# Kernel tuning notes

Hardware: AMD Instinct MI355X
Metric: run time of the kernel (lower is better)

Reference implementation:

```python
import jax, jax.numpy as jnp
import numpy as np

B, C_IN, H, W = 4, 1536, 64, 64   # SGI input: cat of three 512-ch encoder maps at 64x64
HID, OUT = 1536, 512
N = H * W


def _grid_edge_index(h, w):
    # 4-connected bidirectional grid, matching SGI.grid_edge_index
    idx = np.arange(h * w).reshape(h, w)
    right = np.stack([idx[:, :-1].ravel(), idx[:, 1:].ravel()])
    down = np.stack([idx[:-1, :].ravel(), idx[1:, :].ravel()])
    ei = np.concatenate([right, down, right[::-1], down[::-1]], axis=1)
    return ei.astype(np.int32)


def setup_inputs() -> dict:
    key = jax.random.key(0)
    ks = jax.random.split(key, 7)
    ei = _grid_edge_index(H, W)
    s = 0.02
    return {
        "x":  jax.random.normal(ks[0], (B, C_IN, H, W), jnp.float32),
        "W1": jax.random.normal(ks[1], (C_IN, HID), jnp.float32) * s,
        "b1": jnp.zeros((HID,), jnp.float32),
        "W2": jax.random.normal(ks[2], (HID, OUT), jnp.float32) * s,
        "b2": jnp.zeros((OUT,), jnp.float32),
        "Wl": jax.random.normal(ks[3], (C_IN, OUT), jnp.float32) * s,
        "bl": jnp.zeros((OUT,), jnp.float32),
        "src": jnp.asarray(ei[0]),
        "dst": jnp.asarray(ei[1]),
    }


def _gcn(h_in, Wt, b, src, dst, inv_sqrt_deg, inv_deg):
    # PyG GCNConv: lin -> symmetric-normalized aggregation (with self loops) -> +bias
    h = h_in @ Wt                                   # [B, N, F]
    norm = inv_sqrt_deg[src] * inv_sqrt_deg[dst]    # [E]
    msgs = h[:, src, :] * norm[None, :, None]       # [B, E, F]
    # self-loop contribution has norm 1/deg_i
    agg = (h * inv_deg[None, :, None]).at[:, dst, :].add(msgs)
    return agg + b


def reference(x, W1, b1, W2, b2, Wl, bl, src, dst):
    Bb, C, Hh, Ww = x.shape
    n = Hh * Ww
    # degree including self loop (graph is symmetric)
    deg = jnp.zeros((n,), x.dtype).at[dst].add(1.0) + 1.0
    inv_sqrt_deg = jax.lax.rsqrt(deg)
    inv_deg = 1.0 / deg

    xt = x.reshape(Bb, C, n).transpose(0, 2, 1)     # [B, N, C]
    identity = xt
    origin = xt @ Wl + bl                           # [B, N, OUT]
    h = jax.nn.relu(_gcn(xt, W1, b1, src, dst, inv_sqrt_deg, inv_deg))
    h = _gcn(h + identity, W2, b2, src, dst, inv_sqrt_deg, inv_deg)
    out = h * origin                                # [B, N, OUT]
    return out.transpose(0, 2, 1).reshape(Bb, out.shape[-1], Hh, Ww)
```

## Files before the change

### kernel.cpp

```cpp
#include <hip/hip_runtime.h>
#include <hip/hip_bf16.h>
#include <stdint.h>


typedef __bf16 bf16;
typedef float f32x4 __attribute__((ext_vector_type(4)));
typedef bf16 bf16x8 __attribute__((ext_vector_type(8)));

#define NB 4
#define NN 4096
#define CIN 1536
#define HIDF 1536
#define OUTF 512

__device__ __forceinline__ float degree_of(int n) {
  const int x = n & 63, y = n >> 6;
  return 1.0f + (x > 0) + (x < 63) + (y > 0) + (y < 63);
}
__device__ __forceinline__ float deg2(int gx, int gy) {
  return 1.0f + (gx > 0) + (gx < 63) + (gy > 0) + (gy < 63);
}

#define XBLK 6144
#define W1BLK 576
#define W2BLK 192

__global__ __launch_bounds__(256) void prep(
    const float* __restrict__ x, const float* __restrict__ W1,
    const float* __restrict__ W2, const float* __restrict__ Wl,
    bf16* __restrict__ xt, bf16* __restrict__ xa, bf16* __restrict__ w1t,
    bf16* __restrict__ w2t, bf16* __restrict__ wlt) {
  __shared__ float vt[64 * 64];
  __shared__ float at[64 * 64];
  const int B = blockIdx.x, t = threadIdx.x;
  const int tx = t & 15, ty = t >> 4;
  const int lane = t & 63, w = t >> 6;
  const int u = lane & 7, n3 = lane >> 3;

  if (B < XBLK) {
    const int slot = B >> 3;
    const int nt = (B & 7) * 8 + (slot & 7);
    const int ct = (slot >> 3) % 24;
    const int bb = (slot >> 3) / 24;
    const int gy = nt;
    const int n0 = nt * 64, c0 = ct * 64;
    const float* xb = x + (long)bb * CIN * NN;
#pragma unroll
    for (int cc = 0; cc < 4; cc++) {
      const int cl = ty * 4 + cc;
      const float* row = xb + (long)(c0 + cl) * NN + n0;
      const int nb = tx * 4;
      f32x4 v = *(const f32x4*)(row + nb);
      f32x4 up = {0.f, 0.f, 0.f, 0.f};
      f32x4 dn = {0.f, 0.f, 0.f, 0.f};
      if (gy > 0) up = *(const f32x4*)(row + nb - 64);
      if (gy < 63) dn = *(const f32x4*)(row + nb + 64);
      const float lf = (tx > 0) ? row[nb - 1] : 0.f;
      const float rt = (tx < 15) ? row[nb + 4] : 0.f;
      f32x4 a;
#pragma unroll
      for (int i = 0; i < 4; i++) {
        const int gx = nb + i;
        const float degn = deg2(gx, gy);
        float s = v[i] * (1.0f / degn);
        const float lv = (i == 0) ? lf : v[i - 1];
        const float rv = (i == 3) ? rt : v[i + 1];
        if (gx > 0) s += lv * rsqrtf(degn * deg2(gx - 1, gy));
        if (gx < 63) s += rv * rsqrtf(degn * deg2(gx + 1, gy));
        if (gy > 0) s += up[i] * rsqrtf(degn * deg2(gx, gy - 1));
        if (gy < 63) s += dn[i] * rsqrtf(degn * deg2(gx, gy + 1));
        a[i] = s;
      }
      const int chunk = tx ^ (2 * ((cl >> 3) & 7));
      *(f32x4*)&vt[cl * 64 + chunk * 4] = v;
      *(f32x4*)&at[cl * 64 + chunk * 4] = a;
    }
    __syncthreads();
    bf16* xtb = xt + (long)bb * NN * CIN;
    bf16* xab = xa + (long)bb * NN * CIN;
#pragma unroll
    for (int q = 0; q < 4; q++) {
      const int j = q * 4 + w;
      const int arr = j & 1, r = j >> 1;
      const int nl = n3 + 8 * r;
      const float* s = arr ? at : vt;
      bf16x8 o;
#pragma unroll
      for (int jj = 0; jj < 8; jj++) {
        const int cl = u * 8 + jj;
        const int col = nl ^ (8 * ((cl >> 3) & 7));
        o[jj] = (bf16)s[cl * 64 + col];
      }
      bf16* outp = arr ? xab : xtb;
      *(bf16x8*)&outp[(long)(n0 + nl) * CIN + c0 + u * 8] = o;
    }
  } else {
    int B2 = B - XBLK;
    const float* srcp;
    bf16* dstp;
    int Fdim, Kd, nt, ct;
    if (B2 < W1BLK) {
      nt = B2 / 24; ct = B2 % 24; srcp = W1; dstp = w1t; Fdim = HIDF; Kd = CIN;
    } else if (B2 < W1BLK + W2BLK) {
      const int l = B2 - W1BLK;
      nt = l / 24; ct = l % 24; srcp = W2; dstp = w2t; Fdim = OUTF; Kd = HIDF;
    } else {
      const int l = B2 - W1BLK - W2BLK;
      nt = l / 24; ct = l % 24; srcp = Wl; dstp = wlt; Fdim = OUTF; Kd = CIN;
    }
    const int n0 = nt * 64, c0 = ct * 64;
#pragma unroll
    for (int cc = 0; cc < 4; cc++) {
      const int cl = ty * 4 + cc;
      const float* row = srcp + (long)(c0 + cl) * Fdim + n0;
      f32x4 v = *(const f32x4*)(row + tx * 4);
      const int chunk = tx ^ (2 * ((cl >> 3) & 7));
      *(f32x4*)&vt[cl * 64 + chunk * 4] = v;
    }
    __syncthreads();
#pragma unroll
    for (int q = 0; q < 2; q++) {
      const int r = q * 4 + w;
      const int nl = n3 + 8 * r;
      bf16x8 o;
#pragma unroll
      for (int jj = 0; jj < 8; jj++) {
        const int cl = u * 8 + jj;
        const int col = nl ^ (8 * ((cl >> 3) & 7));
        o[jj] = (bf16)vt[cl * 64 + col];
      }
      *(bf16x8*)&dstp[(long)(n0 + nl) * Kd + c0 + u * 8] = o;
    }
  }
}

__device__ __forceinline__ void async_copy16(const void* g, void* l) {
  __builtin_amdgcn_global_load_lds(
      (const __attribute__((address_space(1))) void*)g,
      (__attribute__((address_space(3))) void*)l, 16, 0, 0);
}

struct GemmCtx {
  f32x4 acc[4][4];
  int wave, lane, wm, wn, quad, l15;
};

__device__ __forceinline__ void gemm_init(GemmCtx& cx, int t) {
  cx.wave = t >> 6;
  cx.lane = t & 63;
  cx.wm = (cx.wave & 1) * 64;
  cx.wn = (cx.wave >> 1) * 64;
  cx.quad = cx.lane >> 4;
  cx.l15 = cx.lane & 15;
#pragma unroll
  for (int i = 0; i < 4; i++)
#pragma unroll
    for (int j = 0; j < 4; j++) cx.acc[i][j] = {0.f, 0.f, 0.f, 0.f};
}

template <int K>
__device__ __forceinline__ void gemm_kloop(GemmCtx& cx, const bf16* Ab,
                                           const bf16* Bb, bf16* As,
                                           bf16* Bs) {
  const int r = cx.lane >> 3, c8 = cx.lane & 7;
  const int fchunk = c8 ^ r;
  for (int kt = 0; kt < K; kt += 64) {
#pragma unroll
    for (int i = 0; i < 4; i++) {
      const int row = i * 32 + cx.wave * 8;
      async_copy16(Ab + (long)(row + r) * K + kt + fchunk * 8, &As[row * 64]);
      async_copy16(Bb + (long)(row + r) * K + kt + fchunk * 8, &Bs[row * 64]);
    }
    __syncthreads();
#pragma unroll
    for (int kk = 0; kk < 2; kk++) {
      const int q = kk * 4 + cx.quad;
      bf16x8 af[4], bfv[4];
#pragma unroll
      for (int mr = 0; mr < 4; mr++) {
        const int m = cx.wm + mr * 16 + cx.l15;
        af[mr] = *(const bf16x8*)&As[m * 64 + (q ^ (m & 7)) * 8];
      }
#pragma unroll
      for (int nc = 0; nc < 4; nc++) {
        const int n = cx.wn + nc * 16 + cx.l15;
        bfv[nc] = *(const bf16x8*)&Bs[n * 64 + (q ^ (n & 7)) * 8];
      }
#pragma unroll
      for (int mr = 0; mr < 4; mr++)
#pragma unroll
        for (int nc = 0; nc < 4; nc++)
          cx.acc[mr][nc] = __builtin_amdgcn_mfma_f32_16x16x32_bf16(
              af[mr], bfv[nc], cx.acc[mr][nc], 0, 0, 0);
    }
    __syncthreads();
  }
}

__global__ __launch_bounds__(256) void gemm_h(
    const bf16* __restrict__ xa, const bf16* __restrict__ w1t,
    const bf16* __restrict__ xt, bf16* __restrict__ h,
    const float* __restrict__ b1) {
  __shared__ bf16 As[128 * 64];
  __shared__ bf16 Bs[128 * 64];
  GemmCtx cx;
  gemm_init(cx, threadIdx.x);
  const int m0 = blockIdx.x * 128, n0 = blockIdx.y * 128, z = blockIdx.z;
  gemm_kloop<CIN>(cx, xa + (long)z * NN * CIN + (long)m0 * CIN,
                  w1t + (long)n0 * CIN, As, Bs);
  const bf16* Xb = xt + (long)z * NN * HIDF;
  bf16* Cb = h + (long)z * NN * HIDF;
#pragma unroll
  for (int mr = 0; mr < 4; mr++)
#pragma unroll
    for (int nc = 0; nc < 4; nc++) {
      const int gn = n0 + cx.wn + nc * 16 + cx.l15;
      const float bv = b1[gn];
#pragma unroll
      for (int j = 0; j < 4; j++) {
        const int gm = m0 + cx.wm + mr * 16 + cx.quad * 4 + j;
        float v = cx.acc[mr][nc][j] + bv;
        v = v > 0.f ? v : 0.f;
        Cb[(long)gm * HIDF + gn] = (bf16)(v + (float)Xb[(long)gm * HIDF + gn]);
      }
    }
}

template <bool ADD_BIAS>
__global__ __launch_bounds__(256) void gemm_f32(
    const bf16* __restrict__ A, const bf16* __restrict__ Bw,
    float* __restrict__ C, const float* __restrict__ bias) {
  __shared__ bf16 As[128 * 64];
  __shared__ bf16 Bs[128 * 64];
  GemmCtx cx;
  gemm_init(cx, threadIdx.x);
  const int m0 = blockIdx.x * 128, n0 = blockIdx.y * 128, z = blockIdx.z;
  gemm_kloop<CIN>(cx, A + (long)z * NN * CIN + (long)m0 * CIN,
                  Bw + (long)n0 * CIN, As, Bs);
  float* Cb = C + (long)z * NN * OUTF;
#pragma unroll
  for (int mr = 0; mr < 4; mr++)
#pragma unroll
    for (int nc = 0; nc < 4; nc++) {
      const int gn = n0 + cx.wn + nc * 16 + cx.l15;
      float bv = 0.f;
      if (ADD_BIAS) bv = bias[gn];
#pragma unroll
      for (int j = 0; j < 4; j++) {
        const int gm = m0 + cx.wm + mr * 16 + cx.quad * 4 + j;
        Cb[(long)gm * OUTF + gn] = cx.acc[mr][nc][j] + bv;
      }
    }
}

__global__ __launch_bounds__(256) void stencil2(
    const float* __restrict__ G2, const float* __restrict__ Orig,
    const float* __restrict__ b2, float* __restrict__ out) {
  __shared__ float tile[16][513];
  const int blk = blockIdx.x;
  const int s = ((blk & 7) << 5) + (blk >> 3);
  const int n0 = s * 16, b = blockIdx.y;
  const int t = threadIdx.x;
  const int fq = t & 127, nl = t >> 7;
  const int f = fq * 4;
  const f32x4 bv = *(const f32x4*)(b2 + f);
#pragma unroll
  for (int p = 0; p < 8; p++) {
    const int nLoc = p * 2 + nl;
    const int n = n0 + nLoc;
    const int gx = n & 63, gy = n >> 6;
    const float degn = degree_of(n);
    const float ws = 1.0f / degn;
    const long rb = ((long)b * NN + n) * (long)OUTF + f;
    f32x4 g = *(const f32x4*)(G2 + rb);
    f32x4 a;
#pragma unroll
    for (int i = 0; i < 4; i++) a[i] = g[i] * ws;
    if (gx > 0) {
      const float w = rsqrtf(degn * degree_of(n - 1));
      f32x4 u = *(const f32x4*)(G2 + rb - OUTF);
#pragma unroll
      for (int i = 0; i < 4; i++) a[i] += u[i] * w;
    }
    if (gx < 63) {
      const float w = rsqrtf(degn * degree_of(n + 1));
      f32x4 u = *(const f32x4*)(G2 + rb + OUTF);
#pragma unroll
      for (int i = 0; i < 4; i++) a[i] += u[i] * w;
    }
    if (gy > 0) {
      const float w = rsqrtf(degn * degree_of(n - 64));
      f32x4 u = *(const f32x4*)(G2 + rb - 64L * OUTF);
#pragma unroll
      for (int i = 0; i < 4; i++) a[i] += u[i] * w;
    }
    if (gy < 63) {
      const float w = rsqrtf(degn * degree_of(n + 64));
      f32x4 u = *(const f32x4*)(G2 + rb + 64L * OUTF);
#pragma unroll
      for (int i = 0; i < 4; i++) a[i] += u[i] * w;
    }
    f32x4 og = *(const f32x4*)(Orig + rb);
#pragma unroll
    for (int i = 0; i < 4; i++) tile[nLoc][f + i] = (a[i] + bv[i]) * og[i];
  }
  __syncthreads();
  const int nl2 = t & 15, f0 = t >> 4;
#pragma unroll
  for (int q = 0; q < 32; q++) {
    const int ff = q * 16 + f0;
    out[((long)b * OUTF + ff) * (long)NN + n0 + nl2] = tile[nl2][ff];
  }
}

extern "C" void kernel_launch(void* const* d_in, const int* in_sizes, int n_in,
                              void* d_out, int out_size, void* d_ws,
                              size_t ws_size, hipStream_t stream) {
  const float* x = (const float*)d_in[0];
  const float* W1 = (const float*)d_in[1];
  const float* b1 = (const float*)d_in[2];
  const float* W2 = (const float*)d_in[3];
  const float* b2 = (const float*)d_in[4];
  const float* Wl = (const float*)d_in[5];
  const float* bl = (const float*)d_in[6];
  float* out = (float*)d_out;

  uint8_t* ws = (uint8_t*)d_ws;
  size_t off = 0;
  auto alloc = [&](size_t bytes) -> void* {
    void* p = ws + off;
    off += (bytes + 255) & ~(size_t)255;
    return p;
  };
  bf16* xt = (bf16*)alloc((size_t)NB * NN * CIN * 2);
  bf16* xa = (bf16*)alloc((size_t)NB * NN * CIN * 2);
  bf16* hb = (bf16*)alloc((size_t)NB * NN * HIDF * 2);
  bf16* w1t = (bf16*)alloc((size_t)HIDF * CIN * 2);
  bf16* w2t = (bf16*)alloc((size_t)OUTF * HIDF * 2);
  bf16* wlt = (bf16*)alloc((size_t)OUTF * CIN * 2);
  float* origin = (float*)xa;
  float* g2 = (float*)xt;

  prep<<<XBLK + W1BLK + 2 * W2BLK, 256, 0, stream>>>(x, W1, W2, Wl, xt, xa,
                                                     w1t, w2t, wlt);
  gemm_h<<<dim3(NN / 128, HIDF / 128, NB), 256, 0, stream>>>(xa, w1t, xt, hb,
                                                             b1);
  gemm_f32<true><<<dim3(NN / 128, OUTF / 128, NB), 256, 0, stream>>>(
      xt, wlt, origin, bl);
  gemm_f32<false><<<dim3(NN / 128, OUTF / 128, NB), 256, 0, stream>>>(
      hb, w2t, g2, nullptr);
  stencil2<<<dim3(256, NB), 256, 0, stream>>>(g2, origin, b2, out);
}
```

Baseline: 385.3 us.

## Rewrite first GEMM as 256x256 double-buffered, phase-scheduled MFMA kernel

Replaces the 128x128 tile first-layer GEMM with a 256x256 tile, 512-thread kernel. Its LDS is double-buffered, global-to-LDS async copies are interleaved into four MFMA phases with explicit barriers, waitcnt and priority hints, and blocks are remapped over a flattened grid. The batch dimension is folded into M since rows are contiguous across batches. The aim is higher arithmetic intensity and overlap of loads with compute. In exchange it uses more registers and LDS, so occupancy is lower, and the hand-written scheduling is fragile.

```diff
diff --git a/kernel.cpp b/kernel.cpp
--- a/kernel.cpp
+++ b/kernel.cpp
@@ -197,34 +197,170 @@
   }
 }
 
-__global__ __launch_bounds__(256) void gemm_h(
+#define TS (256 * 64)
+
+__device__ __forceinline__ void stage64(const bf16* g, bf16* l, int rowbase,
+                                        int r, int fc, int kt) {
+  async_copy16(g + (long)(rowbase + r) * CIN + kt + fc, &l[rowbase * 64]);
+}
+
+#define LDA(mh)                                                           \
+  {                                                                       \
+    _Pragma("unroll") for (int kk = 0; kk < 2; kk++) {                    \
+      _Pragma("unroll") for (int mr = 0; mr < 4; mr++) {                  \
+        const int m = wm + (mh) * 64 + mr * 16 + l15;                     \
+        const int q = kk * 4 + quad;                                      \
+        af[kk][mr] = *(const bf16x8*)&As[m * 64 + ((q ^ (m & 7)) * 8)];   \
+      }                                                                   \
+    }                                                                     \
+  }
+
+#define LDB(dst, nh)                                                      \
+  {                                                                       \
+    _Pragma("unroll") for (int kk = 0; kk < 2; kk++) {                    \
+      _Pragma("unroll") for (int nc = 0; nc < 2; nc++) {                  \
+        const int n = wn + (nh) * 32 + nc * 16 + l15;                     \
+        const int q = kk * 4 + quad;                                      \
+        dst[kk][nc] = *(const bf16x8*)&Bs[n * 64 + ((q ^ (n & 7)) * 8)];  \
+      }                                                                   \
+    }                                                                     \
+  }
+
+#define PHASE_MFMA(mh, nh, BF)                                            \
+  {                                                                       \
+    _Pragma("unroll") for (int kk = 0; kk < 2; kk++) {                    \
+      _Pragma("unroll") for (int mr = 0; mr < 4; mr++) {                  \
+        _Pragma("unroll") for (int nc = 0; nc < 2; nc++) {                \
+          acc[(mh) * 4 + mr][(nh) * 2 + nc] =                             \
+              __builtin_amdgcn_mfma_f32_16x16x32_bf16(                    \
+                  af[kk][mr], BF[kk][nc],                                 \
+                  acc[(mh) * 4 + mr][(nh) * 2 + nc], 0, 0, 0);            \
+        }                                                                 \
+      }                                                                   \
+    }                                                                     \
+  }
+
+#define PH_ENTER()                                  \
+  __builtin_amdgcn_s_barrier();                     \
+  asm volatile("s_waitcnt lgkmcnt(0)" ::: "memory");\
+  __builtin_amdgcn_sched_barrier(0);                \
+  __builtin_amdgcn_s_setprio(1);
+
+#define PH_EXIT()                                   \
+  __builtin_amdgcn_s_setprio(0);                    \
+  __builtin_amdgcn_sched_barrier(0);                \
+  asm volatile("s_waitcnt vmcnt(4)" ::: "memory");  \
+  __builtin_amdgcn_s_barrier();                     \
+  __builtin_amdgcn_sched_barrier(0);
+
+__global__ __launch_bounds__(512) void gemm_h256(
     const bf16* __restrict__ xa, const bf16* __restrict__ w1t,
     const bf16* __restrict__ xt, bf16* __restrict__ h,
     const float* __restrict__ b1) {
-  __shared__ bf16 As[128 * 64];
-  __shared__ bf16 Bs[128 * 64];
-  GemmCtx cx;
-  gemm_init(cx, threadIdx.x);
-  const int m0 = blockIdx.x * 128, n0 = blockIdx.y * 128, z = blockIdx.z;
-  gemm_kloop<CIN>(cx, xa + (long)z * NN * CIN + (long)m0 * CIN,
-                  w1t + (long)n0 * CIN, As, Bs);
-  const bf16* Xb = xt + (long)z * NN * HIDF;
-  bf16* Cb = h + (long)z * NN * HIDF;
-#pragma unroll
-  for (int mr = 0; mr < 4; mr++)
-#pragma unroll
-    for (int nc = 0; nc < 4; nc++) {
-      const int gn = n0 + cx.wn + nc * 16 + cx.l15;
+  __shared__ bf16 sA[2 * TS];
+  __shared__ bf16 sB[2 * TS];
+  const int t = threadIdx.x;
+  const int wave = t >> 6, lane = t & 63;
+  const int quad = lane >> 4, l15 = lane & 15;
+  const int wm = (wave >> 2) * 128, wn = (wave & 3) * 64;
+  const int r = lane >> 3, c8 = lane & 7;
+  const int fc = (c8 ^ r) * 8;
+  const int w8 = wave * 8;
+  const int brow = (wave >> 2) * 64 + (wave & 3) * 8;
+
+  const int bid = blockIdx.x;
+  const int s = (bid & 7) * 48 + (bid >> 3);
+  const int mt = s & 63, nt = s >> 6;
+  const int m0 = mt * 256, n0 = nt * 256;
+
+  const bf16* Ag = xa + (long)m0 * CIN;
+  const bf16* Bg = w1t + (long)n0 * CIN;
+
+  f32x4 acc[8][4];
+#pragma unroll
+  for (int i = 0; i < 8; i++)
+#pragma unroll
+    for (int j = 0; j < 4; j++) acc[i][j] = {0.f, 0.f, 0.f, 0.f};
+
+  bf16x8 af[2][4], bf0[2][2], bf1[2][2];
+
+  stage64(Ag, sA, w8, r, fc, 0);
+  stage64(Ag, sA, 128 + w8, r, fc, 0);
+  stage64(Bg, sB, brow, r, fc, 0);
+  stage64(Bg, sB, 128 + brow, r, fc, 0);
+  stage64(Bg, sB, brow + 32, r, fc, 0);
+  stage64(Bg, sB, 128 + brow + 32, r, fc, 0);
+  stage64(Ag, sA, 64 + w8, r, fc, 0);
+  stage64(Ag, sA, 192 + w8, r, fc, 0);
+  asm volatile("s_waitcnt vmcnt(0)" ::: "memory");
+  __builtin_amdgcn_s_barrier();
+  __builtin_amdgcn_sched_barrier(0);
+
+  const int NT = CIN / 64;
+#pragma unroll 2
+  for (int tt = 0; tt < NT; ++tt) {
+    const int cu = tt & 1;
+    const bf16* As = sA + cu * TS;
+    const bf16* Bs = sB + cu * TS;
+    bf16* Ad = sA + (cu ^ 1) * TS;
+    bf16* Bd = sB + (cu ^ 1) * TS;
+    const int ktn = ((tt + 1 < NT) ? (tt + 1) : tt) * 64;
+
+    LDA(0);
+    LDB(bf0, 0);
+    stage64(Ag, Ad, w8, r, fc, ktn);
+    stage64(Ag, Ad, 128 + w8, r, fc, ktn);
+    PH_ENTER();
+    PHASE_MFMA(0, 0, bf0);
+    PH_EXIT();
+
+    LDB(bf1, 1);
+    stage64(Bg, Bd, brow, r, fc, ktn);
+    stage64(Bg, Bd, 128 + brow, r, fc, ktn);
+    PH_ENTER();
+    PHASE_MFMA(0, 1, bf1);
+    PH_EXIT();
+
+    LDA(1);
+    stage64(Bg, Bd, brow + 32, r, fc, ktn);
+    stage64(Bg, Bd, 128 + brow + 32, r, fc, ktn);
+    PH_ENTER();
+    PHASE_MFMA(1, 1, bf1);
+    PH_EXIT();
+
+    stage64(Ag, Ad, 64 + w8, r, fc, ktn);
+    stage64(Ag, Ad, 192 + w8, r, fc, ktn);
+    __builtin_amdgcn_s_barrier();
+    __builtin_amdgcn_sched_barrier(0);
+    __builtin_amdgcn_s_setprio(1);
+    PHASE_MFMA(1, 0, bf0);
+    PH_EXIT();
+  }
+
+#pragma unroll
+  for (int MR = 0; MR < 8; MR++) {
+    const int mbase = m0 + wm + (MR >> 2) * 64 + (MR & 3) * 16 + quad * 4;
+#pragma unroll
+    for (int NC = 0; NC < 4; NC++) {
+      const int gn = n0 + wn + (NC >> 1) * 32 + (NC & 1) * 16 + l15;
       const float bv = b1[gn];
 #pragma unroll
       for (int j = 0; j < 4; j++) {
-        const int gm = m0 + cx.wm + mr * 16 + cx.quad * 4 + j;
-        float v = cx.acc[mr][nc][j] + bv;
+        const int gm = mbase + j;
+        float v = acc[MR][NC][j] + bv;
         v = v > 0.f ? v : 0.f;
-        Cb[(long)gm * HIDF + gn] = (bf16)(v + (float)Xb[(long)gm * HIDF + gn]);
-      }
-    }
-}
+        h[(long)gm * HIDF + gn] =
+            (bf16)(v + (float)xt[(long)gm * HIDF + gn]);
+      }
+    }
+  }
+}
+
+#undef LDA
+#undef LDB
+#undef PHASE_MFMA
+#undef PH_ENTER
+#undef PH_EXIT
 
 template <bool ADD_BIAS>
 __global__ __launch_bounds__(256) void gemm_f32(
@@ -343,8 +479,8 @@
 
   prep<<<XBLK + W1BLK + 2 * W2BLK, 256, 0, stream>>>(x, W1, W2, Wl, xt, xa,
                                                      w1t, w2t, wlt);
-  gemm_h<<<dim3(NN / 128, HIDF / 128, NB), 256, 0, stream>>>(xa, w1t, xt, hb,
-                                                             b1);
+  gemm_h256<<<dim3((NN * NB / 256) * (HIDF / 256)), 512, 0, stream>>>(
+      xa, w1t, xt, hb, b1);
   gemm_f32<true><<<dim3(NN / 128, OUTF / 128, NB), 256, 0, stream>>>(
       xt, wlt, origin, bl);
   gemm_f32<false><<<dim3(NN / 128, OUTF / 128, NB), 256, 0, stream>>>(
```

Measured after the change: 392.9 us. Within noise of the previous version (+2.0%).

## Fuse hidden and origin GEMMs into one launch with LDS-staged vector epilogues

Applied to the files above, without the earlier changes.

Merges the first GCN GEMM and the origin (Wl) GEMM into a single grid of 2048 blocks. Block id picks which GEMM a block runs, and origin gets its own workspace buffer when space allows, so the two can share one launch. All GEMM epilogues now stage accumulators through swizzled shared memory and write coalesced 16-byte vectors instead of scattered scalar stores. This aims to cut launch and tail-wave overhead and uncoalesced writes, at the cost of extra LDS round-trips and syncs plus more workspace.

```diff
diff --git a/kernel.cpp b/kernel.cpp
--- a/kernel.cpp
+++ b/kernel.cpp
@@ -197,60 +197,131 @@
   }
 }
 
-__global__ __launch_bounds__(256) void gemm_h(
+__device__ __forceinline__ void bounce_write(const GemmCtx& cx, float* stg,
+                                             int half) {
+  if ((cx.wn >> 6) == half) {
+#pragma unroll
+    for (int mr = 0; mr < 4; mr++)
+#pragma unroll
+      for (int nc = 0; nc < 4; nc++)
+#pragma unroll
+        for (int j = 0; j < 4; j++) {
+          const int row = cx.wm + mr * 16 + cx.quad * 4 + j;
+          const int col = nc * 16 + cx.l15;
+          stg[row * 64 + (col ^ ((row & 7) << 2))] = cx.acc[mr][nc][j];
+        }
+  }
+}
+
+__global__ __launch_bounds__(256) void gemm_ho(
     const bf16* __restrict__ xa, const bf16* __restrict__ w1t,
-    const bf16* __restrict__ xt, bf16* __restrict__ h,
-    const float* __restrict__ b1) {
-  __shared__ bf16 As[128 * 64];
-  __shared__ bf16 Bs[128 * 64];
+    const bf16* __restrict__ xt, bf16* __restrict__ hb,
+    const float* __restrict__ b1, const bf16* __restrict__ wlt,
+    float* __restrict__ origin, const float* __restrict__ bl, int base) {
+  __shared__ float stg[128 * 64];
+  bf16* As = (bf16*)stg;
+  bf16* Bs = (bf16*)&stg[4096];
+  GemmCtx cx;
+  gemm_init(cx, threadIdx.x);
+  const int id = blockIdx.x + base;
+  const int t = threadIdx.x;
+  const int r2 = t >> 1, cb = (t & 1) * 32;
+  const int sh = (r2 & 7) << 2;
+
+  if (id < 1536) {
+    const int m0 = (id & 31) * 128;
+    const int yz = id >> 5;
+    const int n0 = (yz % 12) * 128;
+    const int z = yz / 12;
+    gemm_kloop<CIN>(cx, xa + (long)z * NN * CIN + (long)m0 * CIN,
+                    w1t + (long)n0 * CIN, As, Bs);
+    const bf16* Xb = xt + (long)z * NN * HIDF;
+    bf16* Cb = hb + (long)z * NN * HIDF;
+#pragma unroll
+    for (int half = 0; half < 2; half++) {
+      if (half) __syncthreads();
+      bounce_write(cx, stg, half);
+      __syncthreads();
+      const int gnb = n0 + half * 64 + cb;
+      const long rowoff = (long)(m0 + r2) * HIDF + gnb;
+#pragma unroll
+      for (int q = 0; q < 4; q++) {
+        const int c0 = cb + q * 8;
+        const f32x4 v0 = *(const f32x4*)&stg[r2 * 64 + (c0 ^ sh)];
+        const f32x4 v1 = *(const f32x4*)&stg[r2 * 64 + ((c0 + 4) ^ sh)];
+        const f32x4 bv0 = *(const f32x4*)&b1[gnb + q * 8];
+        const f32x4 bv1 = *(const f32x4*)&b1[gnb + q * 8 + 4];
+        const bf16x8 xv = *(const bf16x8*)&Xb[rowoff + q * 8];
+        bf16x8 ov;
+#pragma unroll
+        for (int i = 0; i < 4; i++) {
+          float a = v0[i] + bv0[i];
+          a = a > 0.f ? a : 0.f;
+          ov[i] = (bf16)(a + (float)xv[i]);
+          float c = v1[i] + bv1[i];
+          c = c > 0.f ? c : 0.f;
+          ov[i + 4] = (bf16)(c + (float)xv[i + 4]);
+        }
+        *(bf16x8*)&Cb[rowoff + q * 8] = ov;
+      }
+    }
+  } else {
+    const int o = id - 1536;
+    const int m0 = (o & 31) * 128;
+    const int yz = o >> 5;
+    const int n0 = (yz & 3) * 128;
+    const int z = yz >> 2;
+    gemm_kloop<CIN>(cx, xt + (long)z * NN * CIN + (long)m0 * CIN,
+                    wlt + (long)n0 * CIN, As, Bs);
+    float* Cb = origin + (long)z * NN * OUTF;
+#pragma unroll
+    for (int half = 0; half < 2; half++) {
+      if (half) __syncthreads();
+      bounce_write(cx, stg, half);
+      __syncthreads();
+      const int gnb = n0 + half * 64 + cb;
+      const long rowoff = (long)(m0 + r2) * OUTF + gnb;
+#pragma unroll
+      for (int q = 0; q < 8; q++) {
+        const int c0 = cb + q * 4;
+        f32x4 v = *(const f32x4*)&stg[r2 * 64 + (c0 ^ sh)];
+        const f32x4 bv = *(const f32x4*)&bl[gnb + q * 4];
+#pragma unroll
+        for (int i = 0; i < 4; i++) v[i] += bv[i];
+        *(f32x4*)&Cb[rowoff + q * 4] = v;
+      }
+    }
+  }
+}
+
+__global__ __launch_bounds__(256) void gemm2k(const bf16* __restrict__ A,
+                                              const bf16* __restrict__ Bw,
+                                              float* __restrict__ C) {
+  __shared__ float stg[128 * 64];
+  bf16* As = (bf16*)stg;
+  bf16* Bs = (bf16*)&stg[4096];
   GemmCtx cx;
   gemm_init(cx, threadIdx.x);
   const int m0 = blockIdx.x * 128, n0 = blockIdx.y * 128, z = blockIdx.z;
-  gemm_kloop<CIN>(cx, xa + (long)z * NN * CIN + (long)m0 * CIN,
-                  w1t + (long)n0 * CIN, As, Bs);
-  const bf16* Xb = xt + (long)z * NN * HIDF;
-  bf16* Cb = h + (long)z * NN * HIDF;
-#pragma unroll
-  for (int mr = 0; mr < 4; mr++)
-#pragma unroll
-    for (int nc = 0; nc < 4; nc++) {
-      const int gn = n0 + cx.wn + nc * 16 + cx.l15;
-      const float bv = b1[gn];
-#pragma unroll
-      for (int j = 0; j < 4; j++) {
-        const int gm = m0 + cx.wm + mr * 16 + cx.quad * 4 + j;
-        float v = cx.acc[mr][nc][j] + bv;
-        v = v > 0.f ? v : 0.f;
-        Cb[(long)gm * HIDF + gn] = (bf16)(v + (float)Xb[(long)gm * HIDF + gn]);
-      }
-    }
-}
-
-template <bool ADD_BIAS>
-__global__ __launch_bounds__(256) void gemm_f32(
-    const bf16* __restrict__ A, const bf16* __restrict__ Bw,
-    float* __restrict__ C, const float* __restrict__ bias) {
-  __shared__ bf16 As[128 * 64];
-  __shared__ bf16 Bs[128 * 64];
-  GemmCtx cx;
-  gemm_init(cx, threadIdx.x);
-  const int m0 = blockIdx.x * 128, n0 = blockIdx.y * 128, z = blockIdx.z;
-  gemm_kloop<CIN>(cx, A + (long)z * NN * CIN + (long)m0 * CIN,
-                  Bw + (long)n0 * CIN, As, Bs);
+  gemm_kloop<HIDF>(cx, A + (long)z * NN * HIDF + (long)m0 * HIDF,
+                   Bw + (long)n0 * HIDF, As, Bs);
   float* Cb = C + (long)z * NN * OUTF;
-#pragma unroll
-  for (int mr = 0; mr < 4; mr++)
-#pragma unroll
-    for (int nc = 0; nc < 4; nc++) {
-      const int gn = n0 + cx.wn + nc * 16 + cx.l15;
-      float bv = 0.f;
-      if (ADD_BIAS) bv = bias[gn];
-#pragma unroll
-      for (int j = 0; j < 4; j++) {
-        const int gm = m0 + cx.wm + mr * 16 + cx.quad * 4 + j;
-        Cb[(long)gm * OUTF + gn] = cx.acc[mr][nc][j] + bv;
-      }
-    }
+  const int t = threadIdx.x;
+  const int r2 = t >> 1, cb = (t & 1) * 32;
+  const int sh = (r2 & 7) << 2;
+#pragma unroll
+  for (int half = 0; half < 2; half++) {
+    if (half) __syncthreads();
+    bounce_write(cx, stg, half);
+    __syncthreads();
+    const long rowoff = (long)(m0 + r2) * OUTF + n0 + half * 64 + cb;
+#pragma unroll
+    for (int q = 0; q < 8; q++) {
+      const int c0 = cb + q * 4;
+      const f32x4 v = *(const f32x4*)&stg[r2 * 64 + (c0 ^ sh)];
+      *(f32x4*)&Cb[rowoff + q * 4] = v;
+    }
+  }
 }
 
 __global__ __launch_bounds__(256) void stencil2(
@@ -338,16 +409,26 @@
   bf16* w1t = (bf16*)alloc((size_t)HIDF * CIN * 2);
   bf16* w2t = (bf16*)alloc((size_t)OUTF * HIDF * 2);
   bf16* wlt = (bf16*)alloc((size_t)OUTF * CIN * 2);
-  float* origin = (float*)xa;
-  float* g2 = (float*)xt;
+  const size_t base_need = off;
+  float* origin_ded = (float*)alloc((size_t)NB * NN * OUTF * 4);
+  const size_t fused_need = off;
 
   prep<<<XBLK + W1BLK + 2 * W2BLK, 256, 0, stream>>>(x, W1, W2, Wl, xt, xa,
                                                      w1t, w2t, wlt);
-  gemm_h<<<dim3(NN / 128, HIDF / 128, NB), 256, 0, stream>>>(xa, w1t, xt, hb,
-                                                             b1);
-  gemm_f32<true><<<dim3(NN / 128, OUTF / 128, NB), 256, 0, stream>>>(
-      xt, wlt, origin, bl);
-  gemm_f32<false><<<dim3(NN / 128, OUTF / 128, NB), 256, 0, stream>>>(
-      hb, w2t, g2, nullptr);
-  stencil2<<<dim3(256, NB), 256, 0, stream>>>(g2, origin, b2, out);
-}
+  if (ws_size >= fused_need) {
+    float* origin = origin_ded;
+    float* g2 = (float*)xa;
+    gemm_ho<<<2048, 256, 0, stream>>>(xa, w1t, xt, hb, b1, wlt, origin, bl, 0);
+    gemm2k<<<dim3(32, 4, 4), 256, 0, stream>>>(hb, w2t, g2);
+    stencil2<<<dim3(256, NB), 256, 0, stream>>>(g2, origin, b2, out);
+  } else {
+    (void)base_need;
+    float* origin = (float*)xa;
+    float* g2 = (float*)xt;
+    gemm_ho<<<1536, 256, 0, stream>>>(xa, w1t, xt, hb, b1, wlt, origin, bl, 0);
+    gemm_ho<<<512, 256, 0, stream>>>(xa, w1t, xt, hb, b1, wlt, origin, bl,
+                                     1536);
+    gemm2k<<<dim3(32, 4, 4), 256, 0, stream>>>(hb, w2t, g2);
+    stencil2<<<dim3(256, NB), 256, 0, stream>>>(g2, origin, b2, out);
+  }
+}
```

New measurement: 405.9 us. 1.05x slower.

## Double-buffer LDS tiles in GEMM k-loop to overlap async loads with MFMA

Applied to the files above, without the earlier changes.

Doubles the shared-memory A and B tiles and issues the async copy for tile t+1 while computing on tile t, so that global-to-LDS latency overlaps with MFMA work instead of stalling on a barrier before every tile. This doubles LDS use per block to 64KB, which may reduce occupancy. The last iteration redundantly reloads the final tile into the other buffer, and the per-iteration synchronization sits in the hidden part of the loop body.

```diff
diff --git a/kernel.cpp b/kernel.cpp
--- a/kernel.cpp
+++ b/kernel.cpp
@@ -164,14 +164,27 @@
                                            bf16* Bs) {
   const int r = cx.lane >> 3, c8 = cx.lane & 7;
   const int fchunk = c8 ^ r;
-  for (int kt = 0; kt < K; kt += 64) {
+  constexpr int NT = K / 64;
+#pragma unroll
+  for (int i = 0; i < 4; i++) {
+    const int row = i * 32 + cx.wave * 8;
+    async_copy16(Ab + (long)(row + r) * K + fchunk * 8, &As[row * 64]);
+    async_copy16(Bb + (long)(row + r) * K + fchunk * 8, &Bs[row * 64]);
+  }
+  __syncthreads();
+#pragma unroll 2
+  for (int t = 0; t < NT; ++t) {
+    const int cur = (t & 1) * (128 * 64);
+    const int nxt = cur ^ (128 * 64);
+    const int ktn = ((t + 1 < NT) ? t + 1 : t) * 64;
 #pragma unroll
     for (int i = 0; i < 4; i++) {
       const int row = i * 32 + cx.wave * 8;
-      async_copy16(Ab + (long)(row + r) * K + kt + fchunk * 8, &As[row * 64]);
-      async_copy16(Bb + (long)(row + r) * K + kt + fchunk * 8, &Bs[row * 64]);
-    }
-    __syncthreads();
+      async_copy16(Ab + (long)(row + r) * K + ktn + fchunk * 8,
+                   &As[nxt + row * 64]);
+      async_copy16(Bb + (long)(row + r) * K + ktn + fchunk * 8,
+                   &Bs[nxt + row * 64]);
+    }
 #pragma unroll
     for (int kk = 0; kk < 2; kk++) {
       const int q = kk * 4 + cx.quad;
@@ -179,12 +192,12 @@
 #pragma unroll
       for (int mr = 0; mr < 4; mr++) {
         const int m = cx.wm + mr * 16 + cx.l15;
-        af[mr] = *(const bf16x8*)&As[m * 64 + (q ^ (m & 7)) * 8];
+        af[mr] = *(const bf16x8*)&As[cur + m * 64 + (q ^ (m & 7)) * 8];
       }
 #pragma unroll
       for (int nc = 0; nc < 4; nc++) {
         const int n = cx.wn + nc * 16 + cx.l15;
-        bfv[nc] = *(const bf16x8*)&Bs[n * 64 + (q ^ (n & 7)) * 8];
+        bfv[nc] = *(const bf16x8*)&Bs[cur + n * 64 + (q ^ (n & 7)) * 8];
       }
 #pragma unroll
       for (int mr = 0; mr < 4; mr++)
@@ -201,8 +214,8 @@
     const bf16* __restrict__ xa, const bf16* __restrict__ w1t,
     const bf16* __restrict__ xt, bf16* __restrict__ h,
     const float* __restrict__ b1) {
-  __shared__ bf16 As[128 * 64];
-  __shared__ bf16 Bs[128 * 64];
+  __shared__ bf16 As[2 * 128 * 64];
+  __shared__ bf16 Bs[2 * 128 * 64];
   GemmCtx cx;
   gemm_init(cx, threadIdx.x);
   const int m0 = blockIdx.x * 128, n0 = blockIdx.y * 128, z = blockIdx.z;
@@ -230,8 +243,8 @@
 __global__ __launch_bounds__(256) void gemm_f32(
     const bf16* __restrict__ A, const bf16* __restrict__ Bw,
     float* __restrict__ C, const float* __restrict__ bias) {
-  __shared__ bf16 As[128 * 64];
-  __shared__ bf16 Bs[128 * 64];
+  __shared__ bf16 As[2 * 128 * 64];
+  __shared__ bf16 Bs[2 * 128 * 64];
   GemmCtx cx;
   gemm_init(cx, threadIdx.x);
   const int m0 = blockIdx.x * 128, n0 = blockIdx.y * 128, z = blockIdx.z;
```

After: 366.5 us. 1.05x faster.
